# Kernel tuning notes

Hardware: AMD Instinct MI355X
Metric: run time of the kernel (lower is better)

## Reference

```python
import jax, jax.numpy as jnp
import numpy as np

DIM = 1024
DEPTH = 6
HEADS = 8
FF_MULT = 4
LN_EPS = 1e-5
LEAKY_SLOPE = 0.01


def _layernorm(x, w, b):
    m = jnp.mean(x, axis=-1, keepdims=True)
    v = jnp.mean(jnp.square(x - m), axis=-1, keepdims=True)
    return (x - m) * jax.lax.rsqrt(v + LN_EPS) * w + b


def setup_inputs() -> dict:
    key = jax.random.key(0)
    ks = jax.random.split(key, 12)
    b, t = 2, 4096
    s = 0.02  # weight init scale
    return {
        "x": jax.random.normal(ks[0], (b, t, DIM), dtype=jnp.float32),
        "ln1_w": jnp.ones((DEPTH, DIM), jnp.float32),
        "ln1_b": jnp.zeros((DEPTH, DIM), jnp.float32),
        "wq": jax.random.normal(ks[1], (DEPTH, DIM, DIM), jnp.float32) * s,
        "wk": jax.random.normal(ks[2], (DEPTH, DIM, DIM), jnp.float32) * s,
        "wv": jax.random.normal(ks[3], (DEPTH, DIM, DIM), jnp.float32) * s,
        "wo": jax.random.normal(ks[4], (DEPTH, DIM, DIM), jnp.float32) * s,
        "bo": jnp.zeros((DEPTH, DIM), jnp.float32),
        "ln2_w": jnp.ones((DEPTH, DIM), jnp.float32),
        "ln2_b": jnp.zeros((DEPTH, DIM), jnp.float32),
        "w1": jax.random.normal(ks[5], (DEPTH, DIM, FF_MULT * DIM), jnp.float32) * s,
        "w2": jax.random.normal(ks[6], (DEPTH, FF_MULT * DIM, DIM), jnp.float32) * s,
    }


def _linear_attn(q, k, v):
    # q,k,v: [b,h,n,d]; non-causal kernelized linear attention
    q = jax.nn.softmax(q, axis=-1)        # over feature dim d
    k = jax.nn.softmax(k, axis=-2)        # over sequence dim n
    context = jnp.einsum('bhnd,bhne->bhde', k, v)
    return jnp.einsum('bhnd,bhde->bhne', q, context)


def reference(x, ln1_w, ln1_b, wq, wk, wv, wo, bo, ln2_w, ln2_b, w1, w2):
    b, t, e = x.shape
    h, dh = HEADS, e // HEADS
    for i in range(DEPTH):
        # PreNorm + SelfAttention + residual
        xn = _layernorm(x, ln1_w[i], ln1_b[i])
        q = (xn @ wq[i]).reshape(b, t, h, dh).transpose(0, 2, 1, 3)
        k = (xn @ wk[i]).reshape(b, t, h, dh).transpose(0, 2, 1, 3)
        v = (xn @ wv[i]).reshape(b, t, h, dh).transpose(0, 2, 1, 3)
        attn = _linear_attn(q, k, v)                      # [b,h,t,dh]
        attn = attn.transpose(0, 2, 1, 3).reshape(b, t, e)
        x = attn @ wo[i] + bo[i] + x
        # PreNorm + FeedForward + residual
        xn = _layernorm(x, ln2_w[i], ln2_b[i])
        hdn = xn @ w1[i]
        hdn = jnp.where(hdn >= 0, hdn, LEAKY_SLOPE * hdn)  # LeakyReLU(0.01)
        x = hdn @ w2[i] + x
    return x
```

## Files before the change

### kernel.cpp

```cpp
#include <hip/hip_runtime.h>

typedef unsigned short u16;
typedef unsigned int u32;
typedef unsigned long long uptr;

typedef __bf16 bf16x8 __attribute__((ext_vector_type(8)));
typedef float f32x4 __attribute__((ext_vector_type(4)));
typedef u16 u16x8 __attribute__((ext_vector_type(8)));
typedef u16 u16x4 __attribute__((ext_vector_type(4)));
typedef u16 u16x2 __attribute__((ext_vector_type(2)));

static __device__ __forceinline__ u16 f2bf(float f) {
    u32 x = __float_as_uint(f);
    u32 r = x + 0x7fffu + ((x >> 16) & 1u);
    return (u16)(r >> 16);
}
static __device__ __forceinline__ float bf2f(u16 u) {
    return __uint_as_float(((u32)u) << 16);
}

static __device__ __forceinline__ void async_cp16(const u16* g, const u16* lds) {
    __builtin_amdgcn_global_load_lds(
        (__attribute__((address_space(1))) u32*)(uptr)(const void*)g,
        (__attribute__((address_space(3))) u32*)(u32)(uptr)(const void*)lds,
        16, 0, 0);
}

enum { E_F32 = 0, E_BF16 = 1, E_BIASRES = 2, E_LEAKY = 3, E_RES = 4, E_QKV = 5 };

template <int EPI>
__global__ __launch_bounds__(256, 4) void gemm_tn(
    const u16* __restrict__ A, const u16* __restrict__ B, void* __restrict__ C,
    void* __restrict__ C2, void* __restrict__ C3,
    const float* __restrict__ bias, const float* __restrict__ res,
    float* __restrict__ colsum,
    int K, int lda, int ldb, int ldc, int H, int ZS,
    long sAb, long sAh, long sBb, long sBh, long sCb, long sCh, long sCz)
{
    __shared__ u16 smem[EPI == E_QKV ? 17408 : 16384];

    const int tid  = threadIdx.x;
    const int lane = tid & 63;
    const int wid  = tid >> 6;
    const int wm   = (wid >> 1) * 64;
    const int wn   = (wid & 1) * 64;

    const int gx = gridDim.x;
    int lin = blockIdx.x + gx * blockIdx.y;
    const int nwg = gx * gridDim.y;
    if ((nwg & 7) == 0) {
        const int q8 = nwg >> 3;
        lin = (lin & 7) * q8 + (lin >> 3);
    }
    const int n0 = (lin % gx) * 128;
    const int m0 = (lin / gx) * 128;

    const int z    = blockIdx.z;
    const int bb   = z / (H * ZS);
    const int hh   = (z / ZS) % H;
    const int zsp  = z % ZS;

    const u16* Ab = A + bb * sAb + hh * sAh + (long)zsp * K;
    const u16* Bb = B + bb * sBb + hh * sBh + (long)zsp * K;

    const int srow = wid * 32 + (lane >> 2);
    const int skel = ((lane & 3) ^ ((lane >> 3) & 3)) * 8;
    const u16* aS = Ab + (long)(m0 + srow) * lda + skel;
    const u16* bS = Bb + (long)(n0 + srow) * ldb + skel;

    const int cswz = ((lane >> 4) ^ (((lane & 15) >> 1) & 3)) * 8;
    const int aoff = (wm + (lane & 15)) * 32 + cswz;
    const int boff = 4096 + (wn + (lane & 15)) * 32 + cswz;

    f32x4 acc[4][4] = {};

    const int nk = K >> 5;
    auto stage = [&](int t, int bsel) {
        const u16* a0 = aS + t * 32;
        const u16* b0 = bS + t * 32;
        u16* base = smem + bsel * 8192;
        async_cp16(a0,            base + wid * 1024);
        async_cp16(a0 + 16 * lda, base + wid * 1024 + 512);
        async_cp16(b0,            base + 4096 + wid * 1024);
        async_cp16(b0 + 16 * ldb, base + 4096 + wid * 1024 + 512);
    };

    stage(0, 0);
    for (int kt = 0; kt < nk; ++kt) {
        __syncthreads();
        if (kt + 1 < nk) stage(kt + 1, (kt + 1) & 1);
        const u16* bufp = smem + (kt & 1) * 8192;

        bf16x8 af[4], bfg[4];
#pragma unroll
        for (int i = 0; i < 4; ++i) af[i]  = *(const bf16x8*)(bufp + aoff + i * 512);
#pragma unroll
        for (int i = 0; i < 4; ++i) bfg[i] = *(const bf16x8*)(bufp + boff + i * 512);
#pragma unroll
        for (int mi = 0; mi < 4; ++mi)
#pragma unroll
            for (int ni = 0; ni < 4; ++ni)
                acc[mi][ni] = __builtin_amdgcn_mfma_f32_16x16x32_bf16(af[mi], bfg[ni], acc[mi][ni], 0, 0, 0);
    }

    const int r0 = (lane >> 4) * 4;
    const int cc = lane & 15;

    if constexpr (EPI == E_F32 || EPI == E_BIASRES || EPI == E_RES) {
        float* Cf = (float*)C + bb * sCb + hh * sCh + (long)zsp * sCz;
#pragma unroll
        for (int mi = 0; mi < 4; ++mi)
#pragma unroll
            for (int ni = 0; ni < 4; ++ni) {
                const int col = n0 + wn + ni * 16 + cc;
#pragma unroll
                for (int r = 0; r < 4; ++r) {
                    const int row = m0 + wm + mi * 16 + r0 + r;
                    float v = acc[mi][ni][r];
                    if constexpr (EPI == E_BIASRES) v += bias[col] + res[(long)row * ldc + col];
                    if constexpr (EPI == E_RES)     v += res[(long)row * ldc + col];
                    Cf[(long)row * ldc + col] = v;
                }
            }
    } else if constexpr (EPI == E_BF16 || EPI == E_LEAKY) {
        u16* Cb = (u16*)C + bb * sCb + hh * sCh;
#pragma unroll
        for (int mi = 0; mi < 4; ++mi)
#pragma unroll
            for (int ni = 0; ni < 4; ++ni) {
                const int col = n0 + wn + ni * 16 + cc;
#pragma unroll
                for (int r = 0; r < 4; ++r) {
                    const int row = m0 + wm + mi * 16 + r0 + r;
                    float v = acc[mi][ni][r];
                    if constexpr (EPI == E_LEAKY) v = (v >= 0.f) ? v : 0.01f * v;
                    Cb[(long)row * ldc + col] = f2bf(v);
                }
            }
    } else if constexpr (EPI == E_QKV) {
        if (n0 < 1024) {
            u16* Cb = (u16*)C;
#pragma unroll
            for (int mi = 0; mi < 4; ++mi)
#pragma unroll
                for (int ni = 0; ni < 4; ++ni) {
                    const int col = n0 + wn + ni * 16 + cc;
#pragma unroll
                    for (int r = 0; r < 4; ++r) {
                        const int row = m0 + wm + mi * 16 + r0 + r;
                        Cb[(long)row * ldc + col] = f2bf(acc[mi][ni][r]);
                    }
                }
        } else {
            const bool isK = (n0 < 2048);
            const int nb = n0 - (isK ? 1024 : 2048);
            __syncthreads();
#pragma unroll
            for (int mi = 0; mi < 4; ++mi)
#pragma unroll
                for (int ni = 0; ni < 4; ++ni)
#pragma unroll
                    for (int r = 0; r < 4; ++r) {
                        float v = acc[mi][ni][r];
                        if (isK) v = __expf(v);
                        smem[(wn + ni * 16 + cc) * 136 + wm + mi * 16 + r0 + r] = f2bf(v);
                    }
            __syncthreads();
            const int c = tid >> 1, hf = tid & 1;
            const u16* srcp = smem + c * 136 + hf * 64;
            const long base = ((long)(m0 >> 12) * 1024 + nb + c) * 4096 + (m0 & 4095) + hf * 64;
            u16* Ob = (u16*)(isK ? C2 : C3);
            float s = 0.f;
#pragma unroll
            for (int j = 0; j < 8; ++j) {
                u16x8 vv = *(const u16x8*)(srcp + j * 8);
                if (isK) {
#pragma unroll
                    for (int qq = 0; qq < 8; ++qq) s += bf2f(vv[qq]);
                }
                *(u16x8*)(Ob + base + j * 8) = vv;
            }
            if (isK) {
                s += __shfl_xor(s, 1);
                if (hf == 0) atomicAdd(&colsum[(m0 >> 12) * 1024 + nb + c], s);
            }
        }
    }
}

__global__ __launch_bounds__(256) void layernorm_k(
    const float* __restrict__ x, const float* __restrict__ w,
    const float* __restrict__ b, u16* __restrict__ out)
{
    const int row = blockIdx.x, tid = threadIdx.x, lane = tid & 63, wid = tid >> 6;
    float4 v = ((const float4*)x)[row * 256 + tid];
    float s  = v.x + v.y + v.z + v.w;
    float ss = v.x * v.x + v.y * v.y + v.z * v.z + v.w * v.w;
#pragma unroll
    for (int o = 32; o >= 1; o >>= 1) { s += __shfl_xor(s, o); ss += __shfl_xor(ss, o); }
    __shared__ float red[8];
    if (lane == 0) { red[wid] = s; red[4 + wid] = ss; }
    __syncthreads();
    s  = red[0] + red[1] + red[2] + red[3];
    ss = red[4] + red[5] + red[6] + red[7];
    const float mean = s * (1.f / 1024.f);
    const float var  = ss * (1.f / 1024.f) - mean * mean;
    const float rs   = rsqrtf(var + 1e-5f);
    float4 wv = ((const float4*)w)[tid];
    float4 bv = ((const float4*)b)[tid];
    u16x4 o;
    o[0] = f2bf((v.x - mean) * rs * wv.x + bv.x);
    o[1] = f2bf((v.y - mean) * rs * wv.y + bv.y);
    o[2] = f2bf((v.z - mean) * rs * wv.z + bv.z);
    o[3] = f2bf((v.w - mean) * rs * wv.w + bv.w);
    *(u16x4*)(out + (long)row * 1024 + tid * 4) = o;
}

__global__ __launch_bounds__(256) void qsoftmax_k(u16* __restrict__ q)
{
    const int tid = threadIdx.x, lane = tid & 63, wid = tid >> 6;
    const long seg = (long)blockIdx.x * 4 + wid;
    u16* p = q + seg * 128;
    u16x2 raw = *(const u16x2*)(p + lane * 2);
    float a = bf2f(raw[0]), b = bf2f(raw[1]);
    float m = fmaxf(a, b);
#pragma unroll
    for (int o = 32; o >= 1; o >>= 1) m = fmaxf(m, __shfl_xor(m, o));
    float e0 = __expf(a - m), e1 = __expf(b - m);
    float s = e0 + e1;
#pragma unroll
    for (int o = 32; o >= 1; o >>= 1) s += __shfl_xor(s, o);
    const float inv = 1.f / s;
    u16x2 o2; o2[0] = f2bf(e0 * inv); o2[1] = f2bf(e1 * inv);
    *(u16x2*)(p + lane * 2) = o2;
}

__global__ __launch_bounds__(256) void ctxreduce_k(
    const float* __restrict__ part, const float* __restrict__ S, u16* __restrict__ ctxb)
{
    const int idx = blockIdx.x * 256 + threadIdx.x;
    const int bh = idx >> 14;
    const int d  = idx & 127;
    float s = 0.f;
#pragma unroll
    for (int ks = 0; ks < 16; ++ks) s += part[(long)(bh * 16 + ks) * 16384 + (idx & 16383)];
    s /= S[(bh >> 3) * 1024 + (bh & 7) * 128 + d];
    ctxb[idx] = f2bf(s);
}

__global__ __launch_bounds__(256) void transw_k(
    const float* __restrict__ in, u16* __restrict__ out, int R, int C,
    long inZ, long outZ)
{
    __shared__ u16 t[64 * 68];
    const float* inp = in + (long)blockIdx.z * inZ;
    u16* outp = out + (long)blockIdx.z * outZ;
    const int r0 = blockIdx.y * 64, c0 = blockIdx.x * 64;
    const int tid = threadIdx.x;
    const int rr = tid >> 4, c4 = (tid & 15) * 4;
#pragma unroll
    for (int i = 0; i < 4; ++i) {
        const int r = rr + i * 16;
        float4 v = *(const float4*)(inp + (long)(r0 + r) * C + c0 + c4);
        u16x4 h; h[0] = f2bf(v.x); h[1] = f2bf(v.y); h[2] = f2bf(v.z); h[3] = f2bf(v.w);
        *(u16x4*)(t + r * 68 + c4) = h;
    }
    __syncthreads();
    const int c = tid >> 2, rs = (tid & 3) * 16;
    u16x8 o0, o1;
#pragma unroll
    for (int i = 0; i < 8; ++i) o0[i] = t[(rs + i) * 68 + c];
#pragma unroll
    for (int i = 0; i < 8; ++i) o1[i] = t[(rs + 8 + i) * 68 + c];
    u16* dst = outp + (long)(c0 + c) * R + r0 + rs;
    *(u16x8*)dst = o0;
    *(u16x8*)(dst + 8) = o1;
}

extern "C" void kernel_launch(void* const* d_in, const int* in_sizes, int n_in,
                              void* d_out, int out_size, void* d_ws, size_t ws_size,
                              hipStream_t stream)
{
    const float* x0   = (const float*)d_in[0];
    const float* ln1w = (const float*)d_in[1];
    const float* ln1b = (const float*)d_in[2];
    const float* wq   = (const float*)d_in[3];
    const float* wk   = (const float*)d_in[4];
    const float* wv   = (const float*)d_in[5];
    const float* wo   = (const float*)d_in[6];
    const float* bo   = (const float*)d_in[7];
    const float* ln2w = (const float*)d_in[8];
    const float* ln2b = (const float*)d_in[9];
    const float* w1   = (const float*)d_in[10];
    const float* w2   = (const float*)d_in[11];
    float* xout = (float*)d_out;

    char* ws = (char*)d_ws;
    size_t off = 0;
    auto alloc = [&](size_t bytes) -> void* {
        void* p = ws + off;
        off += (bytes + 255) & ~(size_t)255;
        return p;
    };
    u16* wqkvt = (u16*)alloc(6ull * 3072 * 1024 * 2);
    u16* wot   = (u16*)alloc(6ull * 1024 * 1024 * 2);
    u16* w1t   = (u16*)alloc(6ull * 1024 * 4096 * 2);
    u16* w2t   = (u16*)alloc(6ull * 4096 * 1024 * 2);
    u16* xn    = (u16*)alloc(8192ull * 1024 * 2);
    u16* qb    = (u16*)alloc(8192ull * 1024 * 2);
    u16* kt    = (u16*)alloc(8192ull * 1024 * 2);
    u16* vt    = (u16*)alloc(8192ull * 1024 * 2);
    u16* attnb = (u16*)alloc(8192ull * 1024 * 2);
    u16* hdn   = (u16*)alloc(8192ull * 4096 * 2);
    float* part = (float*)alloc(256ull * 16384 * 4);
    u16* ctxb  = (u16*)alloc(262144ull * 2);
    float* Ssum = (float*)alloc(8192);

    const dim3 blk(256);

    transw_k<<<dim3(16, 16, 6), blk, 0, stream>>>(wq, wqkvt,           1024, 1024, 1048576L, 3145728L);
    transw_k<<<dim3(16, 16, 6), blk, 0, stream>>>(wk, wqkvt + 1048576, 1024, 1024, 1048576L, 3145728L);
    transw_k<<<dim3(16, 16, 6), blk, 0, stream>>>(wv, wqkvt + 2097152, 1024, 1024, 1048576L, 3145728L);
    transw_k<<<dim3(16, 16, 6), blk, 0, stream>>>(wo, wot, 1024, 1024, 1048576L, 1048576L);
    transw_k<<<dim3(64, 16, 6), blk, 0, stream>>>(w1, w1t, 1024, 4096, 4194304L, 4194304L);
    transw_k<<<dim3(16, 64, 6), blk, 0, stream>>>(w2, w2t, 4096, 1024, 4194304L, 4194304L);

    for (int L = 0; L < 6; ++L) {
        const float* xin = (L == 0) ? x0 : xout;

        layernorm_k<<<8192, blk, 0, stream>>>(xin, ln1w + L * 1024, ln1b + L * 1024, xn);

        hipMemsetAsync(Ssum, 0, 8192, stream);

        gemm_tn<E_QKV><<<dim3(24, 64, 1), blk, 0, stream>>>(
            xn, wqkvt + (size_t)L * 3145728, qb, kt, vt, nullptr, nullptr, Ssum,
            1024, 1024, 1024, 1024, 1, 1, 0, 0, 0, 0, 0, 0, 0);

        qsoftmax_k<<<16384, blk, 0, stream>>>(qb);

        gemm_tn<E_F32><<<dim3(1, 1, 256), blk, 0, stream>>>(
            vt, kt, part, nullptr, nullptr, nullptr, nullptr, nullptr,
            256, 4096, 4096, 128, 8, 16,
            4194304L, 524288L, 4194304L, 524288L, 2097152L, 262144L, 16384L);

        ctxreduce_k<<<1024, blk, 0, stream>>>(part, Ssum, ctxb);

        gemm_tn<E_BF16><<<dim3(1, 32, 16), blk, 0, stream>>>(
            qb, ctxb, attnb, nullptr, nullptr, nullptr, nullptr, nullptr,
            128, 1024, 128, 1024, 8, 1,
            4194304L, 128L, 131072L, 16384L, 4194304L, 128L, 0L);

        gemm_tn<E_BIASRES><<<dim3(8, 64, 1), blk, 0, stream>>>(
            attnb, wot + (size_t)L * 1048576, xout, nullptr, nullptr,
            bo + L * 1024, xin, nullptr,
            1024, 1024, 1024, 1024, 1, 1, 0, 0, 0, 0, 0, 0, 0);

        layernorm_k<<<8192, blk, 0, stream>>>(xout, ln2w + L * 1024, ln2b + L * 1024, xn);

        gemm_tn<E_LEAKY><<<dim3(32, 64, 1), blk, 0, stream>>>(
            xn, w1t + (size_t)L * 4194304, hdn, nullptr, nullptr, nullptr, nullptr, nullptr,
            1024, 1024, 1024, 4096, 1, 1, 0, 0, 0, 0, 0, 0, 0);

        gemm_tn<E_RES><<<dim3(8, 64, 1), blk, 0, stream>>>(
            hdn, w2t + (size_t)L * 4194304, xout, nullptr, nullptr,
            nullptr, xout, nullptr,
            4096, 4096, 4096, 1024, 1, 1, 0, 0, 0, 0, 0, 0, 0);
    }
}
```

Before: 2.370 ms.

## Add 256-row tiled GEMM kernel with swizzled LDS for dense projections

```diff
diff --git a/kernel.cpp b/kernel.cpp
--- a/kernel.cpp
+++ b/kernel.cpp
@@ -28,16 +28,209 @@
 
 enum { E_F32 = 0, E_BF16 = 1, E_BIASRES = 2, E_LEAKY = 3, E_RES = 4, E_QKV = 5 };
 
-template <int EPI>
-__global__ __launch_bounds__(256, 4) void gemm_tn(
+template <int EPI, int BN>
+__global__ __launch_bounds__(512, 2) void gemm256(
     const u16* __restrict__ A, const u16* __restrict__ B, void* __restrict__ C,
     void* __restrict__ C2, void* __restrict__ C3,
     const float* __restrict__ bias, const float* __restrict__ res,
     float* __restrict__ colsum,
+    int K, int lda, int ldb, int ldc)
+{
+    constexpr int WM = (BN == 256) ? 2 : 4;
+    constexpr int WN = (BN == 256) ? 4 : 2;
+    constexpr int MR = 256 / (WM * 16);
+    constexpr int PM = MR / 4;
+    constexpr int BLOADS = BN / 64;
+    constexpr int BBASE = 32768;
+    constexpr int BSTRIDE = BN * 64;
+    __shared__ u16 smem[32768 + 2 * BN * 64];
+
+    const int tid  = threadIdx.x;
+    const int lane = tid & 63;
+    const int wid  = tid >> 6;
+    const int wr   = wid / WN;
+    const int wc   = wid % WN;
+
+    const int gx = gridDim.x;
+    int lin = blockIdx.x + gx * blockIdx.y;
+    {
+        const int q8 = (gx * gridDim.y) >> 3;
+        lin = (lin & 7) * q8 + (lin >> 3);
+    }
+    const int n0 = (lin % gx) * BN;
+    const int m0 = (lin / gx) * 256;
+
+    const int l3  = lane >> 3;
+    const int lch = (lane & 7) ^ l3;
+    const u16* aStage = A + (long)(m0 + wid * 32 + l3) * lda + lch * 8;
+    const u16* bStage = B + (long)(n0 + wid * (BLOADS * 8) + l3) * ldb + lch * 8;
+
+    auto stageT = [&](int t, int b) {
+        const long ko = (long)t * 64;
+        const u16* ap = aStage + ko;
+#pragma unroll
+        for (int j = 0; j < 4; ++j)
+            async_cp16(ap + (long)j * 8 * lda,
+                       smem + b * 16384 + wid * 2048 + j * 512);
+        const u16* bp = bStage + ko;
+#pragma unroll
+        for (int j = 0; j < BLOADS; ++j)
+            async_cp16(bp + (long)j * 8 * ldb,
+                       smem + BBASE + b * BSTRIDE + wid * (BLOADS * 512) + j * 512);
+    };
+
+    const int pch0 = (((lane >> 4)    ) ^ (lane & 7)) * 8;
+    const int pch1 = (((lane >> 4) + 4) ^ (lane & 7)) * 8;
+    const int aFB = (wr * (256 / WM) + (lane & 15)) * 64;
+    const int bFB = (wc * 64 + (lane & 15)) * 64;
+
+    f32x4 acc[MR][4] = {};
+    const int nt = K >> 6;
+
+    stageT(0, 0);
+    stageT(1, 1);
+    if constexpr (BN == 256) asm volatile("s_waitcnt vmcnt(8)" ::: "memory");
+    else                     asm volatile("s_waitcnt vmcnt(6)" ::: "memory");
+    __builtin_amdgcn_s_barrier();
+    __builtin_amdgcn_sched_barrier(0);
+
+    for (int t = 0; t < nt; ++t) {
+        const int cb = t & 1;
+        if (t >= 1 && t + 1 < nt) stageT(t + 1, (t + 1) & 1);
+        __builtin_amdgcn_sched_barrier(0);
+        const u16* aB = smem + cb * 16384 + aFB;
+        const u16* bB = smem + BBASE + cb * BSTRIDE + bFB;
+
+        bf16x8 br[4][2];
+#pragma unroll
+        for (int ni = 0; ni < 4; ++ni) {
+            br[ni][0] = *(const bf16x8*)(bB + ni * 1024 + pch0);
+            br[ni][1] = *(const bf16x8*)(bB + ni * 1024 + pch1);
+        }
+#pragma unroll
+        for (int p = 0; p < 4; ++p) {
+            bf16x8 ar[PM][2];
+#pragma unroll
+            for (int mm = 0; mm < PM; ++mm) {
+                ar[mm][0] = *(const bf16x8*)(aB + (p * PM + mm) * 1024 + pch0);
+                ar[mm][1] = *(const bf16x8*)(aB + (p * PM + mm) * 1024 + pch1);
+            }
+            __builtin_amdgcn_s_setprio(1);
+#pragma unroll
+            for (int mm = 0; mm < PM; ++mm)
+#pragma unroll
+                for (int ni = 0; ni < 4; ++ni) {
+                    acc[p * PM + mm][ni] = __builtin_amdgcn_mfma_f32_16x16x32_bf16(
+                        ar[mm][0], br[ni][0], acc[p * PM + mm][ni], 0, 0, 0);
+                    acc[p * PM + mm][ni] = __builtin_amdgcn_mfma_f32_16x16x32_bf16(
+                        ar[mm][1], br[ni][1], acc[p * PM + mm][ni], 0, 0, 0);
+                }
+            __builtin_amdgcn_s_setprio(0);
+        }
+        asm volatile("s_waitcnt vmcnt(0)" ::: "memory");
+        __builtin_amdgcn_s_barrier();
+        __builtin_amdgcn_sched_barrier(0);
+    }
+
+    const int r0 = (lane >> 4) * 4;
+    const int cc = lane & 15;
+    const int wrows = wr * (256 / WM);
+    const int wcols = wc * 64;
+
+    if constexpr (EPI == E_LEAKY) {
+        u16* Cb = (u16*)C;
+#pragma unroll
+        for (int mi = 0; mi < MR; ++mi)
+#pragma unroll
+            for (int ni = 0; ni < 4; ++ni) {
+                const int col = n0 + wcols + ni * 16 + cc;
+#pragma unroll
+                for (int r = 0; r < 4; ++r) {
+                    const int row = m0 + wrows + mi * 16 + r0 + r;
+                    float v = acc[mi][ni][r];
+                    v = (v >= 0.f) ? v : 0.01f * v;
+                    Cb[(long)row * ldc + col] = f2bf(v);
+                }
+            }
+    } else if constexpr (EPI == E_RES || EPI == E_BIASRES) {
+        float* Cf = (float*)C;
+#pragma unroll
+        for (int mi = 0; mi < MR; ++mi)
+#pragma unroll
+            for (int ni = 0; ni < 4; ++ni) {
+                const int col = n0 + wcols + ni * 16 + cc;
+#pragma unroll
+                for (int r = 0; r < 4; ++r) {
+                    const int row = m0 + wrows + mi * 16 + r0 + r;
+                    float v = acc[mi][ni][r] + res[(long)row * ldc + col];
+                    if constexpr (EPI == E_BIASRES) v += bias[col];
+                    Cf[(long)row * ldc + col] = v;
+                }
+            }
+    } else if constexpr (EPI == E_QKV) {
+        if (n0 < 1024) {
+            u16* Cb = (u16*)C;
+#pragma unroll
+            for (int mi = 0; mi < MR; ++mi)
+#pragma unroll
+                for (int ni = 0; ni < 4; ++ni) {
+                    const int col = n0 + wcols + ni * 16 + cc;
+#pragma unroll
+                    for (int r = 0; r < 4; ++r) {
+                        const int row = m0 + wrows + mi * 16 + r0 + r;
+                        Cb[(long)row * ldc + col] = f2bf(acc[mi][ni][r]);
+                    }
+                }
+        } else {
+            const bool isK = (n0 < 2048);
+            const int nb = n0 - (isK ? 1024 : 2048);
+            __syncthreads();
+#pragma unroll
+            for (int mi = 0; mi < MR; ++mi)
+#pragma unroll
+                for (int ni = 0; ni < 4; ++ni) {
+                    const int col  = wcols + ni * 16 + cc;
+                    const int rowb = wrows + mi * 16 + r0;
+                    const int ch   = rowb >> 3;
+                    u16x4 h;
+#pragma unroll
+                    for (int r = 0; r < 4; ++r) {
+                        float v = acc[mi][ni][r];
+                        if (isK) v = __expf(v);
+                        h[r] = f2bf(v);
+                    }
+                    *(u16x4*)(smem + col * 256 + ((ch ^ (col & 31)) * 8) + (rowb & 7)) = h;
+                }
+            __syncthreads();
+            const int col = tid >> 1, hf = tid & 1;
+            const long gb = ((long)(m0 >> 12) * 1024 + nb + col) * 4096 + (m0 & 4095) + hf * 128;
+            u16* Ob = (u16*)(isK ? C2 : C3);
+            float s = 0.f;
+#pragma unroll
+            for (int c = 0; c < 16; ++c) {
+                const int ch = hf * 16 + c;
+                u16x8 vv = *(const u16x8*)(smem + col * 256 + ((ch ^ (col & 31)) * 8));
+                if (isK) {
+#pragma unroll
+                    for (int q = 0; q < 8; ++q) s += bf2f(vv[q]);
+                }
+                *(u16x8*)(Ob + gb + c * 8) = vv;
+            }
+            if (isK) {
+                s += __shfl_xor(s, 1);
+                if (hf == 0) atomicAdd(&colsum[(m0 >> 12) * 1024 + nb + col], s);
+            }
+        }
+    }
+}
+
+template <int EPI>
+__global__ __launch_bounds__(256, 4) void gemm_tn(
+    const u16* __restrict__ A, const u16* __restrict__ B, void* __restrict__ C,
     int K, int lda, int ldb, int ldc, int H, int ZS,
     long sAb, long sAh, long sBb, long sBh, long sCb, long sCh, long sCz)
 {
-    __shared__ u16 smem[EPI == E_QKV ? 17408 : 16384];
+    __shared__ u16 smem[16384];
 
     const int tid  = threadIdx.x;
     const int lane = tid & 63;
@@ -106,7 +299,7 @@
     const int r0 = (lane >> 4) * 4;
     const int cc = lane & 15;
 
-    if constexpr (EPI == E_F32 || EPI == E_BIASRES || EPI == E_RES) {
+    if constexpr (EPI == E_F32) {
         float* Cf = (float*)C + bb * sCb + hh * sCh + (long)zsp * sCz;
 #pragma unroll
         for (int mi = 0; mi < 4; ++mi)
@@ -116,13 +309,10 @@
 #pragma unroll
                 for (int r = 0; r < 4; ++r) {
                     const int row = m0 + wm + mi * 16 + r0 + r;
-                    float v = acc[mi][ni][r];
-                    if constexpr (EPI == E_BIASRES) v += bias[col] + res[(long)row * ldc + col];
-                    if constexpr (EPI == E_RES)     v += res[(long)row * ldc + col];
-                    Cf[(long)row * ldc + col] = v;
-                }
-            }
-    } else if constexpr (EPI == E_BF16 || EPI == E_LEAKY) {
+                    Cf[(long)row * ldc + col] = acc[mi][ni][r];
+                }
+            }
+    } else if constexpr (EPI == E_BF16) {
         u16* Cb = (u16*)C + bb * sCb + hh * sCh;
 #pragma unroll
         for (int mi = 0; mi < 4; ++mi)
@@ -132,59 +322,9 @@
 #pragma unroll
                 for (int r = 0; r < 4; ++r) {
                     const int row = m0 + wm + mi * 16 + r0 + r;
-                    float v = acc[mi][ni][r];
-                    if constexpr (EPI == E_LEAKY) v = (v >= 0.f) ? v : 0.01f * v;
-                    Cb[(long)row * ldc + col] = f2bf(v);
-                }
-            }
-    } else if constexpr (EPI == E_QKV) {
-        if (n0 < 1024) {
-            u16* Cb = (u16*)C;
-#pragma unroll
-            for (int mi = 0; mi < 4; ++mi)
-#pragma unroll
-                for (int ni = 0; ni < 4; ++ni) {
-                    const int col = n0 + wn + ni * 16 + cc;
-#pragma unroll
-                    for (int r = 0; r < 4; ++r) {
-                        const int row = m0 + wm + mi * 16 + r0 + r;
-                        Cb[(long)row * ldc + col] = f2bf(acc[mi][ni][r]);
-                    }
-                }
-        } else {
-            const bool isK = (n0 < 2048);
-            const int nb = n0 - (isK ? 1024 : 2048);
-            __syncthreads();
-#pragma unroll
-            for (int mi = 0; mi < 4; ++mi)
-#pragma unroll
-                for (int ni = 0; ni < 4; ++ni)
-#pragma unroll
-                    for (int r = 0; r < 4; ++r) {
-                        float v = acc[mi][ni][r];
-                        if (isK) v = __expf(v);
-                        smem[(wn + ni * 16 + cc) * 136 + wm + mi * 16 + r0 + r] = f2bf(v);
-                    }
-            __syncthreads();
-            const int c = tid >> 1, hf = tid & 1;
-            const u16* srcp = smem + c * 136 + hf * 64;
-            const long base = ((long)(m0 >> 12) * 1024 + nb + c) * 4096 + (m0 & 4095) + hf * 64;
-            u16* Ob = (u16*)(isK ? C2 : C3);
-            float s = 0.f;
-#pragma unroll
-            for (int j = 0; j < 8; ++j) {
-                u16x8 vv = *(const u16x8*)(srcp + j * 8);
-                if (isK) {
-#pragma unroll
-                    for (int qq = 0; qq < 8; ++qq) s += bf2f(vv[qq]);
-                }
-                *(u16x8*)(Ob + base + j * 8) = vv;
-            }
-            if (isK) {
-                s += __shfl_xor(s, 1);
-                if (hf == 0) atomicAdd(&colsum[(m0 >> 12) * 1024 + nb + c], s);
-            }
-        }
+                    Cb[(long)row * ldc + col] = f2bf(acc[mi][ni][r]);
+                }
+            }
     }
 }
 
@@ -317,6 +457,7 @@
     float* Ssum = (float*)alloc(8192);
 
     const dim3 blk(256);
+    const dim3 blk5(512);
 
     transw_k<<<dim3(16, 16, 6), blk, 0, stream>>>(wq, wqkvt,           1024, 1024, 1048576L, 3145728L);
     transw_k<<<dim3(16, 16, 6), blk, 0, stream>>>(wk, wqkvt + 1048576, 1024, 1024, 1048576L, 3145728L);
@@ -332,38 +473,39 @@
 
         hipMemsetAsync(Ssum, 0, 8192, stream);
 
-        gemm_tn<E_QKV><<<dim3(24, 64, 1), blk, 0, stream>>>(
+        gemm256<E_QKV, 256><<<dim3(12, 32), blk5, 0, stream>>>(
             xn, wqkvt + (size_t)L * 3145728, qb, kt, vt, nullptr, nullptr, Ssum,
-            1024, 1024, 1024, 1024, 1, 1, 0, 0, 0, 0, 0, 0, 0);
+            1024, 1024, 1024, 1024);
 
         qsoftmax_k<<<16384, blk, 0, stream>>>(qb);
 
         gemm_tn<E_F32><<<dim3(1, 1, 256), blk, 0, stream>>>(
-            vt, kt, part, nullptr, nullptr, nullptr, nullptr, nullptr,
+            vt, kt, part,
             256, 4096, 4096, 128, 8, 16,
             4194304L, 524288L, 4194304L, 524288L, 2097152L, 262144L, 16384L);
 
         ctxreduce_k<<<1024, blk, 0, stream>>>(part, Ssum, ctxb);
 
         gemm_tn<E_BF16><<<dim3(1, 32, 16), blk, 0, stream>>>(
-            qb, ctxb, attnb, nullptr, nullptr, nullptr, nullptr, nullptr,
+            qb, ctxb, attnb,
             128, 1024, 128, 1024, 8, 1,
             4194304L, 128L, 131072L, 16384L, 4194304L, 128L, 0L);
 
-        gemm_tn<E_BIASRES><<<dim3(8, 64, 1), blk, 0, stream>>>(
+        gemm256<E_BIASRES, 128><<<dim3(8, 32), blk5, 0, stream>>>(
             attnb, wot + (size_t)L * 1048576, xout, nullptr, nullptr,
             bo + L * 1024, xin, nullptr,
-            1024, 1024, 1024, 1024, 1, 1, 0, 0, 0, 0, 0, 0, 0);
+            1024, 1024, 1024, 1024);
 
         layernorm_k<<<8192, blk, 0, stream>>>(xout, ln2w + L * 1024, ln2b + L * 1024, xn);
 
-        gemm_tn<E_LEAKY><<<dim3(32, 64, 1), blk, 0, stream>>>(
-            xn, w1t + (size_t)L * 4194304, hdn, nullptr, nullptr, nullptr, nullptr, nullptr,
-            1024, 1024, 1024, 4096, 1, 1, 0, 0, 0, 0, 0, 0, 0);
-
-        gemm_tn<E_RES><<<dim3(8, 64, 1), blk, 0, stream>>>(
+        gemm256<E_LEAKY, 256><<<dim3(16, 32), blk5, 0, stream>>>(
+            xn, w1t + (size_t)L * 4194304, hdn, nullptr, nullptr,
+            nullptr, nullptr, nullptr,
+            1024, 1024, 1024, 4096);
+
+        gemm256<E_RES, 128><<<dim3(8, 32), blk5, 0, stream>>>(
             hdn, w2t + (size_t)L * 4194304, xout, nullptr, nullptr,
             nullptr, xout, nullptr,
-            4096, 4096, 4096, 1024, 1, 1, 0, 0, 0, 0, 0, 0, 0);
-    }
-}
+            4096, 4096, 4096, 1024);
+    }
+}
```

After: 2.238 ms. 1.06x faster.
